# Kernel tuning notes

Hardware: AMD Instinct MI355X
Metric: run time of the kernel (lower is better)

The kernel has to match this reference:

```python
import jax, jax.numpy as jnp
import numpy as np

EPS_MSG = 1e-7   # GENConv message eps
EPS_LN = 1e-5    # LayerNorm eps

N, F_IN, D, D_OUT = 32768, 64, 512, 128


def setup_inputs() -> dict:
    key = jax.random.key(0)
    ks = jax.random.split(key, 20)
    s = 0.02
    inp = {
        "batch": jax.random.normal(ks[0], (1, N, F_IN), jnp.float32),
        "W_enc": jax.random.normal(ks[1], (F_IN, D), jnp.float32) * s,
        "b_enc": jnp.zeros((D,), jnp.float32),
        "Wf": jax.random.normal(ks[2], (D, D_OUT), jnp.float32) * s,
        "bf": jnp.zeros((D_OUT,), jnp.float32),
    }
    for l in range(2):
        inp[f"t{l}"] = jnp.array(1.0, jnp.float32)           # learnable softmax temperature
        inp[f"W1_{l}"] = jax.random.normal(ks[3 + 6 * l], (D, 2 * D), jnp.float32) * s
        inp[f"b1_{l}"] = jnp.zeros((2 * D,), jnp.float32)
        inp[f"g_{l}"] = jnp.ones((2 * D,), jnp.float32)      # LN gamma
        inp[f"be_{l}"] = jnp.zeros((2 * D,), jnp.float32)    # LN beta
        inp[f"W2_{l}"] = jax.random.normal(ks[4 + 6 * l], (2 * D, D), jnp.float32) * s
        inp[f"b2_{l}"] = jnp.zeros((D,), jnp.float32)
    return inp


def _layer_norm(z, g, b):
    mu = jnp.mean(z, axis=-1, keepdims=True)
    var = jnp.var(z, axis=-1, keepdims=True)
    return (z - mu) * jax.lax.rsqrt(var + EPS_LN) * g + b


def _deepgcn_layer(x, t, W1, b1, g, be, W2, b2):
    # res+ block: h = conv(act(norm(x))); return x + h   (norm is Identity here)
    h = jax.nn.relu(x)                       # [n, d]
    # GENConv with complete graph: msg_j = relu(h_j) + eps (independent of target i)
    m = jax.nn.relu(h) + EPS_MSG             # [n, d]
    alpha = jax.nn.softmax(t * m, axis=0)    # per-channel softmax over all source nodes
    agg = jnp.sum(alpha * m, axis=0)         # [d]  -- identical for every target node
    out = h + agg[None, :]                   # + x_dst residual inside GENConv
    # GENConv MLP: Linear(d,2d) -> LayerNorm -> ReLU -> Linear(2d,d)
    z = jax.nn.relu(_layer_norm(out @ W1 + b1, g, be))
    out = z @ W2 + b2
    return x + out


def reference(batch, W_enc, b_enc, Wf, bf,
              t0, W1_0, b1_0, g_0, be_0, W2_0, b2_0,
              t1, W1_1, b1_1, g_1, be_1, W2_1, b2_1):
    bsz, n, _ = batch.shape
    x = batch.reshape(bsz * n, -1) @ W_enc + b_enc   # node encoder
    x = _deepgcn_layer(x, t0, W1_0, b1_0, g_0, be_0, W2_0, b2_0)
    x = _deepgcn_layer(x, t1, W1_1, b1_1, g_1, be_1, W2_1, b2_1)
    x = jax.nn.relu(x)                               # layers[0].act(layers[0].norm(x)), norm=Identity
    out = x @ Wf + bf
    return out.reshape(bsz, n, -1)
```

## Files before the change

kernel.cpp:

```cpp
#include <hip/hip_runtime.h>

#define DEV __device__ __forceinline__

typedef __attribute__((ext_vector_type(8))) short s8v;
typedef __attribute__((ext_vector_type(4))) float f4v;

DEV short f2bf(float f) {
  unsigned u = __builtin_bit_cast(unsigned, f);
  u += 0x7fffu + ((u >> 16) & 1u);
  return (short)(u >> 16);
}
DEV float bf2f(short s) {
  unsigned u = ((unsigned)(unsigned short)s) << 16;
  return __builtin_bit_cast(float, u);
}

DEV f4v mfma_16x16x32_bf16(s8v a, s8v b, f4v c) {
  asm("v_mfma_f32_16x16x32_bf16 %0, %1, %2, %0" : "+v"(c) : "v"(a), "v"(b));
  return c;
}

DEV s8v relu8(s8v a) {
#pragma unroll
  for (int i = 0; i < 8; ++i) a[i] = a[i] > (short)0 ? a[i] : (short)0;
  return a;
}

__global__ __launch_bounds__(256) void tconv_k(const float* __restrict__ in,
                                               short* __restrict__ out,
                                               int K, int N) {
  __shared__ float t[64][65];
  const int nb = blockIdx.x * 64, kb = blockIdx.y * 64;
  const int c = threadIdx.x & 63, r0 = threadIdx.x >> 6;
#pragma unroll
  for (int rr = 0; rr < 64; rr += 4)
    t[rr + r0][c] = in[(size_t)(kb + rr + r0) * N + nb + c];
  __syncthreads();
#pragma unroll
  for (int rr = 0; rr < 64; rr += 4)
    out[(size_t)(nb + rr + r0) * K + kb + c] = f2bf(t[c][rr + r0]);
}

__global__ __launch_bounds__(256) void conv_k(const float* __restrict__ in,
                                              short* __restrict__ out, int n4) {
  int i = blockIdx.x * 256 + threadIdx.x;
  if (i >= n4) return;
  float4 v = ((const float4*)in)[i];
  short4 o;
  o.x = f2bf(v.x);
  o.y = f2bf(v.y);
  o.z = f2bf(v.z);
  o.w = f2bf(v.w);
  ((short4*)out)[i] = o;
}

__global__ __launch_bounds__(256) void zero_k(float* p, int n) {
  int i = blockIdx.x * 256 + threadIdx.x;
  if (i < n) p[i] = 0.f;
}

__global__ __launch_bounds__(256) void finalize_k(const float* __restrict__ sums,
                                                  const float* __restrict__ W1,
                                                  const float* __restrict__ b1,
                                                  float* __restrict__ biasEff) {
  __shared__ float agg[512];
  __shared__ float part[16][16];
  const int tid = threadIdx.x;
  for (int d = tid; d < 512; d += 256) agg[d] = sums[512 + d] / sums[d];
  __syncthreads();
  const int j = blockIdx.x * 16 + (tid & 15);
  const int grp = tid >> 4;
  float p = 0.f;
#pragma unroll 4
  for (int dd = 0; dd < 32; ++dd) {
    int d = grp * 32 + dd;
    p += agg[d] * W1[(size_t)d * 1024 + j];
  }
  part[grp][tid & 15] = p;
  __syncthreads();
  if (tid < 16) {
    float a = b1[blockIdx.x * 16 + tid];
#pragma unroll
    for (int g = 0; g < 16; ++g) a += part[g][tid];
    biasEff[blockIdx.x * 16 + tid] = a;
  }
}

__global__ __launch_bounds__(256) void ln_relu_k(short* __restrict__ z,
                                                 const float* __restrict__ g,
                                                 const float* __restrict__ be) {
  const int row = blockIdx.x * 4 + (threadIdx.x >> 6);
  const int lane = threadIdx.x & 63;
  short* zr = z + (size_t)row * 1024;
  s8v c0 = *(const s8v*)&zr[lane * 8];
  s8v c1 = *(const s8v*)&zr[512 + lane * 8];
  float v[16];
  float s = 0.f, q = 0.f;
#pragma unroll
  for (int i = 0; i < 8; ++i) { v[i] = bf2f(c0[i]); v[8 + i] = bf2f(c1[i]); }
#pragma unroll
  for (int i = 0; i < 16; ++i) { s += v[i]; q += v[i] * v[i]; }
#pragma unroll
  for (int o = 32; o > 0; o >>= 1) { s += __shfl_xor(s, o); q += __shfl_xor(q, o); }
  float mu = s * (1.f / 1024.f);
  float var = q * (1.f / 1024.f) - mu * mu;
  float rs = rsqrtf(var + 1e-5f);
  float gv[16], bv[16];
#pragma unroll
  for (int i = 0; i < 8; ++i) {
    gv[i] = g[lane * 8 + i];      gv[8 + i] = g[512 + lane * 8 + i];
    bv[i] = be[lane * 8 + i];     bv[8 + i] = be[512 + lane * 8 + i];
  }
  s8v o0, o1;
#pragma unroll
  for (int i = 0; i < 8; ++i) {
    o0[i] = f2bf(fmaxf((v[i] - mu) * rs * gv[i] + bv[i], 0.f));
    o1[i] = f2bf(fmaxf((v[8 + i] - mu) * rs * gv[8 + i] + bv[8 + i], 0.f));
  }
  *(s8v*)&zr[lane * 8] = o0;
  *(s8v*)&zr[512 + lane * 8] = o1;
}

#define F_ADD   1
#define F_WF32  2
#define F_WBF   4
#define F_SM    8
#define F_RELUA 16

#define VM8  asm volatile("s_waitcnt vmcnt(8)" ::: "memory")
#define VM0  asm volatile("s_waitcnt vmcnt(0)" ::: "memory")
#define SBAR __builtin_amdgcn_s_barrier()
#define SCH0 __builtin_amdgcn_sched_barrier(0)

template <int FLAGS>
__global__ __launch_bounds__(256) void gemm_k(const short* __restrict__ A,
                                              const short* __restrict__ Bt,
                                              const float* __restrict__ bias,
                                              const short* __restrict__ Xin,
                                              short* __restrict__ Cb,
                                              float* __restrict__ Cf,
                                              const float* __restrict__ tptr,
                                              float* __restrict__ sums,
                                              int M, int N, int K) {
  __shared__ short lA0[128 * 64];
  __shared__ short lB0[128 * 64];
  __shared__ short lA1[128 * 64];
  __shared__ short lB1[128 * 64];
  const int tid = threadIdx.x;
  const int lane = tid & 63, wid = tid >> 6;
  const int wr = wid >> 1, wc = wid & 1;
  const int nwg = gridDim.x * gridDim.y;
  const int wg = blockIdx.y * gridDim.x + blockIdx.x;
  const int swz = (wg & 7) * (nwg >> 3) + (wg >> 3);
  const int bx = swz % gridDim.x, by = swz / gridDim.x;
  const int brow = by * 128, bcol = bx * 128;
  const int l15 = lane & 15, lhi = lane >> 4;
  f4v acc[4][4] = {};

  auto stage = [&](short* dA, short* dB, int t) {
    const int k0 = t << 6;
#pragma unroll
    for (int r = 0; r < 4; ++r) {
      int chunk = r * 256 + tid;
      int row = chunk >> 3;
      int kc = ((chunk & 7) ^ (row & 7)) << 3;
      const short* ga = A + (size_t)(brow + row) * K + (k0 + kc);
      const short* gb = Bt + (size_t)(bcol + row) * K + (k0 + kc);
      __builtin_amdgcn_global_load_lds(
          (const __attribute__((address_space(1))) void*)ga,
          (__attribute__((address_space(3))) void*)&dA[(r * 256 + wid * 64) * 8],
          16, 0, 0);
      __builtin_amdgcn_global_load_lds(
          (const __attribute__((address_space(1))) void*)gb,
          (__attribute__((address_space(3))) void*)&dB[(r * 256 + wid * 64) * 8],
          16, 0, 0);
    }
  };

  auto compute = [&](const short* lA, const short* lB) {
    __builtin_amdgcn_s_setprio(1);
#pragma unroll
    for (int kk = 0; kk < 2; ++kk) {
      s8v af[4], bfr[4];
#pragma unroll
      for (int i = 0; i < 4; ++i) {
        const int rowA = wr * 64 + i * 16 + l15;
        const int rowB = wc * 64 + i * 16 + l15;
        const int cA = ((kk * 4 + lhi) ^ (rowA & 7)) << 3;
        const int cB = ((kk * 4 + lhi) ^ (rowB & 7)) << 3;
        af[i]  = *(const s8v*)&lA[rowA * 64 + cA];
        bfr[i] = *(const s8v*)&lB[rowB * 64 + cB];
        if (FLAGS & F_RELUA) af[i] = relu8(af[i]);
      }
#pragma unroll
      for (int mi = 0; mi < 4; ++mi)
#pragma unroll
        for (int ni = 0; ni < 4; ++ni)
          acc[mi][ni] = mfma_16x16x32_bf16(af[mi], bfr[ni], acc[mi][ni]);
    }
    __builtin_amdgcn_s_setprio(0);
  };

  const int nt = K >> 6;
  stage(lA0, lB0, 0);
  if (nt > 1) { stage(lA1, lB1, 1); VM8; } else { VM0; }
  SCH0; SBAR;

  for (int t = 0; t < nt; t += 2) {
    compute(lA0, lB0);
    SBAR;
    if (t + 2 < nt) { stage(lA0, lB0, t + 2); VM8; } else { VM0; }
    SCH0; SBAR;
    if (t + 1 < nt) {
      compute(lA1, lB1);
      SBAR;
      if (t + 3 < nt) { stage(lA1, lB1, t + 3); VM8; } else { VM0; }
      SCH0; SBAR;
    }
  }

  const float tv = (FLAGS & F_SM) ? tptr[0] : 0.f;
  float* sred = (float*)lA0;
  if (FLAGS & F_SM) {
    sred[tid] = 0.f;
    __syncthreads();
  }
#pragma unroll
  for (int ni = 0; ni < 4; ++ni) {
    int col = bcol + wc * 64 + ni * 16 + l15;
    float bv = bias[col];
    float se = 0.f, sem = 0.f;
#pragma unroll
    for (int mi = 0; mi < 4; ++mi) {
#pragma unroll
      for (int r = 0; r < 4; ++r) {
        int row = brow + wr * 64 + mi * 16 + lhi * 4 + r;
        size_t idx = (size_t)row * N + col;
        float v = acc[mi][ni][r] + bv;
        if (FLAGS & F_ADD) v += bf2f(Xin[idx]);
        if (FLAGS & F_WF32) Cf[idx] = v;
        if (FLAGS & F_WBF) Cb[idx] = f2bf(v);
        if (FLAGS & F_SM) {
          float m = fmaxf(v, 0.f) + 1e-7f;
          float e = __expf(tv * m);
          se += e;
          sem += e * m;
        }
      }
    }
    if (FLAGS & F_SM) {
      se += __shfl_xor(se, 16);   se += __shfl_xor(se, 32);
      sem += __shfl_xor(sem, 16); sem += __shfl_xor(sem, 32);
      if (lhi == 0) {
        atomicAdd(&sred[wc * 64 + ni * 16 + l15], se);
        atomicAdd(&sred[128 + wc * 64 + ni * 16 + l15], sem);
      }
    }
  }
  if (FLAGS & F_SM) {
    __syncthreads();
    int v = tid >> 7, c = tid & 127;
    atomicAdd(&sums[v * 512 + bcol + c], sred[v * 128 + c]);
  }
}

extern "C" void kernel_launch(void* const* d_in, const int* in_sizes, int n_in,
                              void* d_out, int out_size, void* d_ws,
                              size_t ws_size, hipStream_t stream) {
  (void)in_sizes; (void)n_in; (void)out_size; (void)ws_size;
  const float* batch = (const float*)d_in[0];
  const float* W_enc = (const float*)d_in[1];
  const float* b_enc = (const float*)d_in[2];
  const float* Wf    = (const float*)d_in[3];
  const float* bfv   = (const float*)d_in[4];
  const float* tptr[2] = {(const float*)d_in[5],  (const float*)d_in[12]};
  const float* W1[2]   = {(const float*)d_in[6],  (const float*)d_in[13]};
  const float* b1[2]   = {(const float*)d_in[7],  (const float*)d_in[14]};
  const float* g[2]    = {(const float*)d_in[8],  (const float*)d_in[15]};
  const float* be[2]   = {(const float*)d_in[9],  (const float*)d_in[16]};
  const float* W2[2]   = {(const float*)d_in[10], (const float*)d_in[17]};
  const float* b2[2]   = {(const float*)d_in[11], (const float*)d_in[18]};
  float* out = (float*)d_out;

  const int M = 32768;
  char* ws = (char*)d_ws;
  size_t off = 0;
  auto alloc = [&](size_t bytes) -> char* {
    char* p = ws + off;
    off += (bytes + 255) & ~(size_t)255;
    return p;
  };
  short* xbf    = (short*)alloc((size_t)M * 512 * 2);
  short* zbuf   = (short*)alloc((size_t)M * 1024 * 2);
  short* bbuf   = (short*)alloc((size_t)M * 64 * 2);
  short* wencT  = (short*)alloc(512 * 64 * 2);
  short* w1T0   = (short*)alloc(1024 * 512 * 2);
  short* w2T0   = (short*)alloc(512 * 1024 * 2);
  short* w1T1   = (short*)alloc(1024 * 512 * 2);
  short* w2T1   = (short*)alloc(512 * 1024 * 2);
  short* wfT    = (short*)alloc(128 * 512 * 2);
  float* sums   = (float*)alloc(2 * 1024 * 4);
  float* biasEff= (float*)alloc(1024 * 4);
  short* w1T[2] = {w1T0, w1T1};
  short* w2T[2] = {w2T0, w2T1};

  tconv_k<<<dim3(512 / 64, 64 / 64), 256, 0, stream>>>(W_enc, wencT, 64, 512);
  tconv_k<<<dim3(1024 / 64, 512 / 64), 256, 0, stream>>>(W1[0], w1T[0], 512, 1024);
  tconv_k<<<dim3(512 / 64, 1024 / 64), 256, 0, stream>>>(W2[0], w2T[0], 1024, 512);
  tconv_k<<<dim3(1024 / 64, 512 / 64), 256, 0, stream>>>(W1[1], w1T[1], 512, 1024);
  tconv_k<<<dim3(512 / 64, 1024 / 64), 256, 0, stream>>>(W2[1], w2T[1], 1024, 512);
  tconv_k<<<dim3(128 / 64, 512 / 64), 256, 0, stream>>>(Wf, wfT, 512, 128);

  conv_k<<<(M * 64 / 4 + 255) / 256, 256, 0, stream>>>(batch, bbuf, M * 64 / 4);
  zero_k<<<(2048 + 255) / 256, 256, 0, stream>>>(sums, 2048);

  gemm_k<F_WBF | F_SM><<<dim3(512 / 128, M / 128), 256, 0, stream>>>(
      bbuf, wencT, b_enc, nullptr, xbf, nullptr, tptr[0], sums, M, 512, 64);

  for (int l = 0; l < 2; ++l) {
    finalize_k<<<64, 256, 0, stream>>>(sums + l * 1024, W1[l], b1[l], biasEff);
    gemm_k<F_WBF | F_RELUA><<<dim3(1024 / 128, M / 128), 256, 0, stream>>>(
        xbf, w1T[l], biasEff, nullptr, zbuf, nullptr, nullptr, nullptr,
        M, 1024, 512);
    ln_relu_k<<<M / 4, 256, 0, stream>>>(zbuf, g[l], be[l]);
    if (l == 0) {
      gemm_k<F_ADD | F_WBF | F_SM><<<dim3(512 / 128, M / 128), 256, 0, stream>>>(
          zbuf, w2T[l], b2[l], xbf, xbf, nullptr, tptr[1], sums + 1024,
          M, 512, 1024);
    } else {
      gemm_k<F_ADD | F_WBF><<<dim3(512 / 128, M / 128), 256, 0, stream>>>(
          zbuf, w2T[l], b2[l], xbf, xbf, nullptr, nullptr, nullptr,
          M, 512, 1024);
    }
  }

  gemm_k<F_WF32 | F_RELUA><<<dim3(128 / 128, M / 128), 256, 0, stream>>>(
      xbf, wfT, bfv, nullptr, nullptr, out, nullptr, nullptr, M, 128, 512);
}
```

Baseline: 376.9 us.

## Add 256x256-tile GEMM kernel for the hidden-layer matmuls

Introduces a 512-thread GEMM kernel with 256x256 output tiles and double-buffered LDS staging, and uses it for both MLP matmuls in each layer. Larger tiles raise arithmetic intensity and cut redundant global and LDS operand traffic per MFMA. The original 128-tile kernel, still used for the encoder and final projection, is simplified to a single-buffered loop with plain barriers, dropping its load/compute overlap. The big-tile kernel uses about 128KB of LDS and many accumulator registers, so occupancy is one block per CU, and the grid shrinks to 256–512 blocks.

```diff
diff --git a/kernel.cpp b/kernel.cpp
--- a/kernel.cpp
+++ b/kernel.cpp
@@ -25,6 +25,17 @@
   for (int i = 0; i < 8; ++i) a[i] = a[i] > (short)0 ? a[i] : (short)0;
   return a;
 }
+
+#define F_ADD   1
+#define F_WF32  2
+#define F_WBF   4
+#define F_SM    8
+#define F_RELUA 16
+
+#define VM8  asm volatile("s_waitcnt vmcnt(8)" ::: "memory")
+#define VM0  asm volatile("s_waitcnt vmcnt(0)" ::: "memory")
+#define SBAR __builtin_amdgcn_s_barrier()
+#define SCH0 __builtin_amdgcn_sched_barrier(0)
 
 __global__ __launch_bounds__(256) void tconv_k(const float* __restrict__ in,
                                                short* __restrict__ out,
@@ -121,17 +132,6 @@
   *(s8v*)&zr[512 + lane * 8] = o1;
 }
 
-#define F_ADD   1
-#define F_WF32  2
-#define F_WBF   4
-#define F_SM    8
-#define F_RELUA 16
-
-#define VM8  asm volatile("s_waitcnt vmcnt(8)" ::: "memory")
-#define VM0  asm volatile("s_waitcnt vmcnt(0)" ::: "memory")
-#define SBAR __builtin_amdgcn_s_barrier()
-#define SCH0 __builtin_amdgcn_sched_barrier(0)
-
 template <int FLAGS>
 __global__ __launch_bounds__(256) void gemm_k(const short* __restrict__ A,
                                               const short* __restrict__ Bt,
@@ -142,10 +142,8 @@
                                               const float* __restrict__ tptr,
                                               float* __restrict__ sums,
                                               int M, int N, int K) {
-  __shared__ short lA0[128 * 64];
-  __shared__ short lB0[128 * 64];
-  __shared__ short lA1[128 * 64];
-  __shared__ short lB1[128 * 64];
+  __shared__ short lA[128 * 64];
+  __shared__ short lB[128 * 64];
   const int tid = threadIdx.x;
   const int lane = tid & 63, wid = tid >> 6;
   const int wr = wid >> 1, wc = wid & 1;
@@ -157,8 +155,7 @@
   const int l15 = lane & 15, lhi = lane >> 4;
   f4v acc[4][4] = {};
 
-  auto stage = [&](short* dA, short* dB, int t) {
-    const int k0 = t << 6;
+  for (int k0 = 0; k0 < K; k0 += 64) {
 #pragma unroll
     for (int r = 0; r < 4; ++r) {
       int chunk = r * 256 + tid;
@@ -168,17 +165,14 @@
       const short* gb = Bt + (size_t)(bcol + row) * K + (k0 + kc);
       __builtin_amdgcn_global_load_lds(
           (const __attribute__((address_space(1))) void*)ga,
-          (__attribute__((address_space(3))) void*)&dA[(r * 256 + wid * 64) * 8],
+          (__attribute__((address_space(3))) void*)&lA[(r * 256 + wid * 64) * 8],
           16, 0, 0);
       __builtin_amdgcn_global_load_lds(
           (const __attribute__((address_space(1))) void*)gb,
-          (__attribute__((address_space(3))) void*)&dB[(r * 256 + wid * 64) * 8],
+          (__attribute__((address_space(3))) void*)&lB[(r * 256 + wid * 64) * 8],
           16, 0, 0);
     }
-  };
-
-  auto compute = [&](const short* lA, const short* lB) {
-    __builtin_amdgcn_s_setprio(1);
+    __syncthreads();
 #pragma unroll
     for (int kk = 0; kk < 2; ++kk) {
       s8v af[4], bfr[4];
@@ -198,29 +192,11 @@
         for (int ni = 0; ni < 4; ++ni)
           acc[mi][ni] = mfma_16x16x32_bf16(af[mi], bfr[ni], acc[mi][ni]);
     }
-    __builtin_amdgcn_s_setprio(0);
-  };
-
-  const int nt = K >> 6;
-  stage(lA0, lB0, 0);
-  if (nt > 1) { stage(lA1, lB1, 1); VM8; } else { VM0; }
-  SCH0; SBAR;
-
-  for (int t = 0; t < nt; t += 2) {
-    compute(lA0, lB0);
-    SBAR;
-    if (t + 2 < nt) { stage(lA0, lB0, t + 2); VM8; } else { VM0; }
-    SCH0; SBAR;
-    if (t + 1 < nt) {
-      compute(lA1, lB1);
-      SBAR;
-      if (t + 3 < nt) { stage(lA1, lB1, t + 3); VM8; } else { VM0; }
-      SCH0; SBAR;
-    }
+    __syncthreads();
   }
 
   const float tv = (FLAGS & F_SM) ? tptr[0] : 0.f;
-  float* sred = (float*)lA0;
+  float* sred = (float*)lA;
   if (FLAGS & F_SM) {
     sred[tid] = 0.f;
     __syncthreads();
@@ -261,6 +237,141 @@
     __syncthreads();
     int v = tid >> 7, c = tid & 127;
     atomicAdd(&sums[v * 512 + bcol + c], sred[v * 128 + c]);
+  }
+}
+
+template <int FLAGS>
+__global__ __launch_bounds__(512) void gemm256_k(const short* __restrict__ A,
+                                                 const short* __restrict__ Bt,
+                                                 const float* __restrict__ bias,
+                                                 const short* __restrict__ Xin,
+                                                 short* __restrict__ Cb,
+                                                 float* __restrict__ Cf,
+                                                 const float* __restrict__ tptr,
+                                                 float* __restrict__ sums,
+                                                 int M, int N, int K) {
+  __shared__ short lA0[256 * 64];
+  __shared__ short lB0[256 * 64];
+  __shared__ short lA1[256 * 64];
+  __shared__ short lB1[256 * 64];
+  const int tid = threadIdx.x;
+  const int lane = tid & 63, wid = tid >> 6;
+  const int wr = wid >> 2, wc = wid & 3;
+  const int nwg = gridDim.x * gridDim.y;
+  const int wg = blockIdx.y * gridDim.x + blockIdx.x;
+  const int swz = (wg & 7) * (nwg >> 3) + (wg >> 3);
+  const int bx = swz % gridDim.x, by = swz / gridDim.x;
+  const int brow = by * 256, bcol = bx * 256;
+  const int l15 = lane & 15, lhi = lane >> 4;
+  f4v acc[8][4] = {};
+
+  auto stage = [&](short* dA, short* dB, int t) {
+    const int k0 = t << 6;
+#pragma unroll
+    for (int r = 0; r < 4; ++r) {
+      int chunk = r * 512 + tid;
+      int row = chunk >> 3;
+      int kc = ((chunk & 7) ^ (row & 7)) << 3;
+      const short* ga = A + (size_t)(brow + row) * K + (k0 + kc);
+      const short* gb = Bt + (size_t)(bcol + row) * K + (k0 + kc);
+      __builtin_amdgcn_global_load_lds(
+          (const __attribute__((address_space(1))) void*)ga,
+          (__attribute__((address_space(3))) void*)&dA[(r * 512 + wid * 64) * 8],
+          16, 0, 0);
+      __builtin_amdgcn_global_load_lds(
+          (const __attribute__((address_space(1))) void*)gb,
+          (__attribute__((address_space(3))) void*)&dB[(r * 512 + wid * 64) * 8],
+          16, 0, 0);
+    }
+  };
+
+  auto compute = [&](const short* lA, const short* lB) {
+    __builtin_amdgcn_s_setprio(1);
+#pragma unroll
+    for (int kk = 0; kk < 2; ++kk) {
+      s8v af[8], bfr[4];
+#pragma unroll
+      for (int i = 0; i < 8; ++i) {
+        const int rowA = wr * 128 + i * 16 + l15;
+        const int cA = ((kk * 4 + lhi) ^ (rowA & 7)) << 3;
+        af[i] = *(const s8v*)&lA[rowA * 64 + cA];
+        if (FLAGS & F_RELUA) af[i] = relu8(af[i]);
+      }
+#pragma unroll
+      for (int j = 0; j < 4; ++j) {
+        const int rowB = wc * 64 + j * 16 + l15;
+        const int cB = ((kk * 4 + lhi) ^ (rowB & 7)) << 3;
+        bfr[j] = *(const s8v*)&lB[rowB * 64 + cB];
+      }
+#pragma unroll
+      for (int mi = 0; mi < 8; ++mi)
+#pragma unroll
+        for (int ni = 0; ni < 4; ++ni)
+          acc[mi][ni] = mfma_16x16x32_bf16(af[mi], bfr[ni], acc[mi][ni]);
+    }
+    __builtin_amdgcn_s_setprio(0);
+  };
+
+  const int nt = K >> 6;
+  stage(lA0, lB0, 0);
+  if (nt > 1) { stage(lA1, lB1, 1); VM8; } else { VM0; }
+  SCH0; SBAR;
+
+  for (int t = 0; t < nt; t += 2) {
+    compute(lA0, lB0);
+    SBAR;
+    if (t + 2 < nt) { stage(lA0, lB0, t + 2); VM8; } else { VM0; }
+    SCH0; SBAR;
+    if (t + 1 < nt) {
+      compute(lA1, lB1);
+      SBAR;
+      if (t + 3 < nt) { stage(lA1, lB1, t + 3); VM8; } else { VM0; }
+      SCH0; SBAR;
+    }
+  }
+
+  const float tv = (FLAGS & F_SM) ? tptr[0] : 0.f;
+  float* sred = (float*)lA0;
+  if (FLAGS & F_SM) {
+    sred[tid] = 0.f;
+    __syncthreads();
+  }
+#pragma unroll
+  for (int ni = 0; ni < 4; ++ni) {
+    int col = bcol + wc * 64 + ni * 16 + l15;
+    float bv = bias[col];
+    float se = 0.f, sem = 0.f;
+#pragma unroll
+    for (int mi = 0; mi < 8; ++mi) {
+#pragma unroll
+      for (int r = 0; r < 4; ++r) {
+        int row = brow + wr * 128 + mi * 16 + lhi * 4 + r;
+        size_t idx = (size_t)row * N + col;
+        float v = acc[mi][ni][r] + bv;
+        if (FLAGS & F_ADD) v += bf2f(Xin[idx]);
+        if (FLAGS & F_WF32) Cf[idx] = v;
+        if (FLAGS & F_WBF) Cb[idx] = f2bf(v);
+        if (FLAGS & F_SM) {
+          float m = fmaxf(v, 0.f) + 1e-7f;
+          float e = __expf(tv * m);
+          se += e;
+          sem += e * m;
+        }
+      }
+    }
+    if (FLAGS & F_SM) {
+      se += __shfl_xor(se, 16);   se += __shfl_xor(se, 32);
+      sem += __shfl_xor(sem, 16); sem += __shfl_xor(sem, 32);
+      if (lhi == 0) {
+        atomicAdd(&sred[wc * 64 + ni * 16 + l15], se);
+        atomicAdd(&sred[256 + wc * 64 + ni * 16 + l15], sem);
+      }
+    }
+  }
+  if (FLAGS & F_SM) {
+    __syncthreads();
+    int v = tid >> 8, c = tid & 255;
+    atomicAdd(&sums[v * 512 + bcol + c], sred[v * 256 + c]);
   }
 }
 
@@ -319,16 +430,17 @@
 
   for (int l = 0; l < 2; ++l) {
     finalize_k<<<64, 256, 0, stream>>>(sums + l * 1024, W1[l], b1[l], biasEff);
-    gemm_k<F_WBF | F_RELUA><<<dim3(1024 / 128, M / 128), 256, 0, stream>>>(
+    gemm256_k<F_WBF | F_RELUA><<<dim3(1024 / 256, M / 256), 512, 0, stream>>>(
         xbf, w1T[l], biasEff, nullptr, zbuf, nullptr, nullptr, nullptr,
         M, 1024, 512);
     ln_relu_k<<<M / 4, 256, 0, stream>>>(zbuf, g[l], be[l]);
     if (l == 0) {
-      gemm_k<F_ADD | F_WBF | F_SM><<<dim3(512 / 128, M / 128), 256, 0, stream>>>(
-          zbuf, w2T[l], b2[l], xbf, xbf, nullptr, tptr[1], sums + 1024,
-          M, 512, 1024);
+      gemm256_k<F_ADD | F_WBF | F_SM>
+          <<<dim3(512 / 256, M / 256), 512, 0, stream>>>(
+              zbuf, w2T[l], b2[l], xbf, xbf, nullptr, tptr[1], sums + 1024,
+              M, 512, 1024);
     } else {
-      gemm_k<F_ADD | F_WBF><<<dim3(512 / 128, M / 128), 256, 0, stream>>>(
+      gemm256_k<F_ADD | F_WBF><<<dim3(512 / 256, M / 256), 512, 0, stream>>>(
           zbuf, w2T[l], b2[l], xbf, xbf, nullptr, nullptr, nullptr,
           M, 512, 1024);
     }
```

Result: slower. 415.5 us (+10.2%).
